# Optimization experiments

Hardware: AMD Instinct MI355X
Metric: run time of the kernel (lower is better)

## Reference

```python
import jax, jax.numpy as jnp
import numpy as np

D_MODEL = 1024
NUM_MODULES = 8
MAX_TRANSLATION = 3.0
MAX_ROT_ANGLE = 3.141592653589793


def setup_inputs() -> dict:
    key = jax.random.key(0)
    k1, k2, k3, k4 = jax.random.split(key, 4)
    B, N = 8, 8192
    node_feats = jax.random.normal(k1, (B, N, D_MODEL), jnp.float32)
    coords = jax.random.normal(k2, (B, N, 3), jnp.float32)
    W = jax.random.normal(k3, (NUM_MODULES * 8, D_MODEL), jnp.float32) * (1.0 / np.sqrt(D_MODEL))
    b = jax.random.normal(k4, (NUM_MODULES * 8,), jnp.float32) * 0.01
    return {"node_feats": node_feats, "coords": coords, "W": W, "b": b}


def _normalize(x, eps=1e-12):
    return x / jnp.clip(jnp.linalg.norm(x, axis=-1, keepdims=True), eps)


def _axis_angle_to_quaternion(aa):
    # pytorch3d convention: quat = [cos(theta/2), axis * sin(theta/2)]
    angles = jnp.linalg.norm(aa, axis=-1, keepdims=True)
    half = angles * 0.5
    small = jnp.abs(angles) < 1e-6
    safe_angles = jnp.where(small, 1.0, angles)
    sin_half_over_angle = jnp.where(small, 0.5 - angles * angles / 48.0, jnp.sin(half) / safe_angles)
    return jnp.concatenate([jnp.cos(half), aa * sin_half_over_angle], axis=-1)


def _quat_mul(a, b):
    aw, ax, ay, az = a[..., 0], a[..., 1], a[..., 2], a[..., 3]
    bw, bx, by, bz = b[..., 0], b[..., 1], b[..., 2], b[..., 3]
    ow = aw * bw - ax * bx - ay * by - az * bz
    ox = aw * bx + ax * bw + ay * bz - az * by
    oy = aw * by - ax * bz + ay * bw + az * bx
    oz = aw * bz + ax * by - ay * bx + az * bw
    return jnp.stack([ow, ox, oy, oz], axis=-1)


def _quat_apply(q, p):
    # q: [B,1,4], p: [B,N,3] -> rotate points: im(q * (0,p) * q^-1)
    pq = jnp.concatenate([jnp.zeros_like(p[..., :1]), p], axis=-1)
    q_inv = q * jnp.array([1.0, -1.0, -1.0, -1.0], q.dtype)
    return _quat_mul(_quat_mul(q, pq), q_inv)[..., 1:]


def reference(node_feats, coords, W, b):
    B, N, _ = coords.shape
    params = (node_feats @ W.T + b).reshape(B, N, NUM_MODULES, 8)
    anchor_logits = params[..., 0:1]   # [B,N,M,1]
    select_logits = params[..., 1:2]
    rot_axis = params[..., 2:5]
    trans = params[..., 5:8]

    anchor_w = jax.nn.softmax(anchor_logits, axis=1)      # softmax over N
    select_p = jax.nn.sigmoid(select_logits)

    angles = jnp.linalg.norm(rot_axis, axis=-1, keepdims=True)
    axis_n = _normalize(rot_axis)
    angles = jnp.tanh(angles) * MAX_ROT_ANGLE
    quats = _axis_angle_to_quaternion(axis_n * angles)    # [B,N,M,4]
    trans = jnp.tanh(trans) * MAX_TRANSLATION             # [B,N,M,3]

    xs = (jnp.moveaxis(quats, 2, 0),     # [M,B,N,4]
          jnp.moveaxis(trans, 2, 0),     # [M,B,N,3]
          jnp.moveaxis(anchor_w, 2, 0),  # [M,B,N,1]
          jnp.moveaxis(select_p, 2, 0))  # [M,B,N,1]

    def step(c, per):
        q, t, aw, sp = per
        anchor = jnp.sum(c * aw, axis=1, keepdims=True)               # [B,1,3]
        s = jnp.clip(jnp.sum(sp, axis=1, keepdims=True), 1e-8)        # [B,1,1]
        q_group = _normalize(jnp.sum(q * sp, axis=1, keepdims=True) / s)  # [B,1,4]
        t_group = jnp.sum(t * sp, axis=1, keepdims=True) / s          # [B,1,3]
        moved = _quat_apply(q_group, c - anchor) + anchor + t_group   # [B,N,3]
        return c + sp * (moved - c), None                             # lerp

    out, _ = jax.lax.scan(step, coords, xs)
    return out
```

## Files before the change

kernel.cpp:

```cpp
#include <hip/hip_runtime.h>
#include <hip/hip_bf16.h>
#include <hip/hip_fp16.h>
#include <math.h>

#define D_MODEL 1024
#define NMOD 8
#define BATCH 8
#define NNODE 8192
#define PI_F 3.14159265358979323846f
#define MAXT 3.0f

typedef short bf16x8 __attribute__((ext_vector_type(8)));
typedef float f32x4 __attribute__((ext_vector_type(4)));

__device__ inline unsigned short f2bf(float x) {
    __hip_bfloat16 h = __float2bfloat16(x);
    return __builtin_bit_cast(unsigned short, h);
}
__device__ inline float h2f(unsigned short u) {
    __half h = __builtin_bit_cast(__half, u);
    return __half2float(h);
}
__device__ inline unsigned short f2h(float x) {
    __half h = __float2half(x);
    return __builtin_bit_cast(unsigned short, h);
}

__global__ void pack_b(const float* __restrict__ W, unsigned short* __restrict__ Bpk) {
    int t = blockIdx.x * 256 + threadIdx.x;
    int l  = t & 63;
    int g  = (t >> 6) & 3;
    int ks = t >> 8;
    int j  = g * 16 + (l & 15);
    int k0 = ks * 32 + ((l >> 4) * 8);
    const float* wp = &W[(size_t)j * D_MODEL + k0];
    bf16x8 pack;
    #pragma unroll
    for (int r = 0; r < 8; ++r) pack[r] = (short)f2bf(wp[r]);
    *reinterpret_cast<bf16x8*>(Bpk + (size_t)t * 8) = pack;
}

__global__ __launch_bounds__(256, 4) void gemm_mfma(
    const float* __restrict__ feats, const unsigned short* __restrict__ Bpk,
    const float* __restrict__ bias,
    unsigned int* __restrict__ esp_out,
    float* __restrict__ sums)
{
    __shared__ float pbuf[4][16][68];
    __shared__ float sacc[64];

    const int tid  = threadIdx.x;
    const int lane = tid & 63;
    const int wv   = tid >> 6;

    if (tid < 64) sacc[tid] = 0.f;
    __syncthreads();

    const int mt    = blockIdx.x * 4 + wv;
    const int mbase = mt * 16;
    const float* arow = feats + (size_t)(mbase + (lane & 15)) * D_MODEL + ((lane >> 4) * 8);
    const bf16x8* bp = reinterpret_cast<const bf16x8*>(Bpk);

    f32x4 acc[4];
    #pragma unroll
    for (int g = 0; g < 4; ++g) acc[g] = (f32x4){0.f, 0.f, 0.f, 0.f};

    #pragma unroll 2
    for (int ks = 0; ks < 32; ++ks) {
        const float4 fa = *reinterpret_cast<const float4*>(arow + ks * 32);
        const float4 fb = *reinterpret_cast<const float4*>(arow + ks * 32 + 4);
        float f[8] = {fa.x, fa.y, fa.z, fa.w, fb.x, fb.y, fb.z, fb.w};
        bf16x8 a;
        #pragma unroll
        for (int i = 0; i < 8; ++i) a[i] = (short)f2bf(f[i]);
        #pragma unroll
        for (int g = 0; g < 4; ++g) {
            bf16x8 bh = bp[(ks * 4 + g) * 64 + lane];
            acc[g] = __builtin_amdgcn_mfma_f32_16x16x32_bf16(a, bh, acc[g], 0, 0, 0);
        }
    }

    #pragma unroll
    for (int g = 0; g < 4; ++g) {
        float bj = bias[g * 16 + (lane & 15)];
        #pragma unroll
        for (int r = 0; r < 4; ++r)
            pbuf[wv][(lane >> 4) * 4 + r][g * 16 + (lane & 15)] = acc[g][r] + bj;
    }

    const int b    = mbase >> 13;
    const int nInB = mbase & 8191;

    #pragma unroll
    for (int h = 0; h < 2; ++h) {
        const int node = lane & 15;
        const int m    = (lane >> 4) + 4 * h;
        const float* pa = &pbuf[wv][node][m * 8];
        float al = pa[0], sl = pa[1];
        float ax = pa[2], ay = pa[3], az = pa[4];
        float tx = pa[5], ty = pa[6], tz = pa[7];

        float ew = expf(al);
        float sp = 1.f / (1.f + expf(-sl));

        float n0  = sqrtf(ax * ax + ay * ay + az * az);
        float inv = 1.f / fmaxf(n0, 1e-12f);
        float ang = tanhf(n0) * PI_F;
        float hf  = 0.5f * ang;
        float shoa = (ang < 1e-6f) ? (0.5f - ang * ang * (1.f / 48.f))
                                   : (sinf(hf) / ang);
        float qw = cosf(hf);
        float fac = inv * ang * shoa;
        float qx = ax * fac, qy = ay * fac, qz = az * fac;

        float ttx = tanhf(tx) * MAXT, tty = tanhf(ty) * MAXT, ttz = tanhf(tz) * MAXT;

        size_t base = ((size_t)(b * NMOD + m)) * NNODE + nInB + node;
        esp_out[base] = ((unsigned)f2h(sp) << 16) | (unsigned)f2h(ew);

        float red[8];
        red[0] = sp;
        red[1] = sp * qw; red[2] = sp * qx; red[3] = sp * qy; red[4] = sp * qz;
        red[5] = sp * ttx; red[6] = sp * tty; red[7] = sp * ttz;
        #pragma unroll
        for (int v = 0; v < 8; ++v) {
            #pragma unroll
            for (int o = 1; o < 16; o <<= 1) red[v] += __shfl_xor(red[v], o);
        }
        if ((lane & 15) == 0) {
            #pragma unroll
            for (int v = 0; v < 8; ++v) atomicAdd(&sacc[m * 8 + v], red[v]);
        }
    }
    __syncthreads();
    if (tid < 64) atomicAdd(&sums[b * 64 + tid], sacc[tid]);
}

__global__ __launch_bounds__(1024) void scan_coords(
    const float* __restrict__ coords,
    const unsigned int* __restrict__ esp_in,
    const float* __restrict__ sums, float* __restrict__ out)
{
    const int b   = blockIdx.x;
    const int tid = threadIdx.x;
    const int lane = tid & 63, wid = tid >> 6;
    __shared__ float redbuf[64];
    __shared__ float bcast[4];

    const int n0 = tid * 8;

    float cx[8], cy[8], cz[8];
    {
        float c[24];
        const float4* cp4 = reinterpret_cast<const float4*>(
            &coords[((size_t)b * NNODE + n0) * 3]);
        #pragma unroll
        for (int q = 0; q < 6; ++q) {
            float4 v = cp4[q];
            c[q * 4 + 0] = v.x; c[q * 4 + 1] = v.y;
            c[q * 4 + 2] = v.z; c[q * 4 + 3] = v.w;
        }
        #pragma unroll
        for (int i = 0; i < 8; ++i) { cx[i] = c[3*i]; cy[i] = c[3*i+1]; cz[i] = c[3*i+2]; }
    }

    const uint4* esp4 = reinterpret_cast<const uint4*>(
        &esp_in[(size_t)b * NMOD * NNODE]);
    uint4 cur0 = esp4[(0 * NNODE + n0) >> 2];
    uint4 cur1 = esp4[((0 * NNODE + n0) >> 2) + 1];

    for (int m = 0; m < NMOD; ++m) {
        const int mn = (m + 1 < NMOD) ? m + 1 : m;
        uint4 nxt0 = esp4[(mn * NNODE + n0) >> 2];
        uint4 nxt1 = esp4[((mn * NNODE + n0) >> 2) + 1];

        unsigned pk[8] = {cur0.x, cur0.y, cur0.z, cur0.w, cur1.x, cur1.y, cur1.z, cur1.w};
        float ev[8], spl[8];
        #pragma unroll
        for (int i = 0; i < 8; ++i) {
            ev[i]  = h2f((unsigned short)(pk[i] & 0xFFFFu));
            spl[i] = h2f((unsigned short)(pk[i] >> 16));
        }

        float se = 0.f, sx = 0.f, sy = 0.f, sz = 0.f;
        #pragma unroll
        for (int i = 0; i < 8; ++i) {
            se += ev[i]; sx += ev[i] * cx[i]; sy += ev[i] * cy[i]; sz += ev[i] * cz[i];
        }
        float vals[4] = {se, sx, sy, sz};
        #pragma unroll
        for (int v = 0; v < 4; ++v) {
            float x = vals[v];
            #pragma unroll
            for (int o = 32; o > 0; o >>= 1) x += __shfl_down(x, o);
            if (lane == 0) redbuf[wid * 4 + v] = x;
        }
        __syncthreads();
        if (wid == 0) {
            float x = redbuf[lane];
            x += __shfl_down(x, 32);
            x += __shfl_down(x, 16);
            x += __shfl_down(x, 8);
            x += __shfl_down(x, 4);
            if (lane < 4) bcast[lane] = x;
        }
        __syncthreads();
        const float SE = bcast[0];
        const float AXc = bcast[1] / SE, AYc = bcast[2] / SE, AZc = bcast[3] / SE;

        const float* sm = &sums[((size_t)b * NMOD + m) * 8];
        float s  = fmaxf(sm[0], 1e-8f);
        float qw = sm[1] / s, qx = sm[2] / s, qy = sm[3] / s, qz = sm[4] / s;
        float qn = sqrtf(qw * qw + qx * qx + qy * qy + qz * qz);
        float qi = 1.f / fmaxf(qn, 1e-12f);
        qw *= qi; qx *= qi; qy *= qi; qz *= qi;
        float tgx = sm[5] / s, tgy = sm[6] / s, tgz = sm[7] / s;

        #pragma unroll
        for (int i = 0; i < 8; ++i) {
            float px = cx[i] - AXc, py = cy[i] - AYc, pz = cz[i] - AZc;
            float ux = qy * pz - qz * py;
            float uy = qz * px - qx * pz;
            float uz = qx * py - qy * px;
            float vx = qy * uz - qz * uy;
            float vy = qz * ux - qx * uz;
            float vz = qx * uy - qy * ux;
            float rx = px + 2.f * (qw * ux + vx);
            float ry = py + 2.f * (qw * uy + vy);
            float rz = pz + 2.f * (qw * uz + vz);
            float mx = rx + AXc + tgx, my = ry + AYc + tgy, mz = rz + AZc + tgz;
            float sp = spl[i];
            cx[i] += sp * (mx - cx[i]);
            cy[i] += sp * (my - cy[i]);
            cz[i] += sp * (mz - cz[i]);
        }
        cur0 = nxt0; cur1 = nxt1;
        __syncthreads();
    }

    {
        float c[24];
        #pragma unroll
        for (int i = 0; i < 8; ++i) { c[3*i] = cx[i]; c[3*i+1] = cy[i]; c[3*i+2] = cz[i]; }
        float4* op4 = reinterpret_cast<float4*>(&out[((size_t)b * NNODE + n0) * 3]);
        #pragma unroll
        for (int q = 0; q < 6; ++q)
            op4[q] = make_float4(c[q*4+0], c[q*4+1], c[q*4+2], c[q*4+3]);
    }
}

extern "C" void kernel_launch(void* const* d_in, const int* in_sizes, int n_in,
                              void* d_out, int out_size, void* d_ws, size_t ws_size,
                              hipStream_t stream) {
    const float* feats  = (const float*)d_in[0];
    const float* coords = (const float*)d_in[1];
    const float* W      = (const float*)d_in[2];
    const float* bias   = (const float*)d_in[3];
    float* out = (float*)d_out;

    char* ws = (char*)d_ws;
    unsigned short* Bpk = (unsigned short*)(ws);
    unsigned int* esp   = (unsigned int*)(ws + 262144);
    float* sums         = (float*)(ws + 262144 + 2097152);

    hipMemsetAsync(sums, 0, (size_t)BATCH * NMOD * 8 * sizeof(float), stream);
    pack_b<<<32, 256, 0, stream>>>(W, Bpk);
    gemm_mfma<<<(BATCH * NNODE) / 64, 256, 0, stream>>>(feats, Bpk, bias, esp, sums);
    scan_coords<<<BATCH, 1024, 0, stream>>>(coords, esp, sums, out);
}
```

Before: 104.6 us.

## Stage packed weights in LDS and double-buffer feature loads in larger GEMM blocks

The GEMM kernel now uses 1024-thread blocks. Each block first copies the whole 128KB packed bf16 weight matrix into LDS with global_load_lds, then streams A rows through two register buffers so the next chunk's loads overlap the current chunk's MFMAs. Weight fragments therefore come from LDS instead of repeated global or L2 reads. The price is 128KB of LDS per block, which limits occupancy to one block per CU, plus a large up-front weight load on each of the 256 blocks and many live registers in the double buffer.

```diff
diff --git a/kernel.cpp b/kernel.cpp
--- a/kernel.cpp
+++ b/kernel.cpp
@@ -40,53 +40,93 @@
     *reinterpret_cast<bf16x8*>(Bpk + (size_t)t * 8) = pack;
 }
 
-__global__ __launch_bounds__(256, 4) void gemm_mfma(
+__device__ __forceinline__ void loadg(float4 (&dst)[8], const float* arow, int g4) {
+    #pragma unroll
+    for (int i = 0; i < 4; ++i) {
+        dst[2 * i]     = *reinterpret_cast<const float4*>(arow + (g4 * 4 + i) * 32);
+        dst[2 * i + 1] = *reinterpret_cast<const float4*>(arow + (g4 * 4 + i) * 32 + 4);
+    }
+}
+
+__device__ __forceinline__ void compg(const float4 (&src)[8], int g4,
+                                      const unsigned short* Blds, int lane,
+                                      f32x4 (&acc)[4]) {
+    #pragma unroll
+    for (int i = 0; i < 4; ++i) {
+        float f[8] = {src[2*i].x, src[2*i].y, src[2*i].z, src[2*i].w,
+                      src[2*i+1].x, src[2*i+1].y, src[2*i+1].z, src[2*i+1].w};
+        bf16x8 a;
+        #pragma unroll
+        for (int j = 0; j < 8; ++j) a[j] = (short)f2bf(f[j]);
+        const int ks = g4 * 4 + i;
+        #pragma unroll
+        for (int g = 0; g < 4; ++g) {
+            bf16x8 bh = *reinterpret_cast<const bf16x8*>(
+                Blds + ((size_t)((ks * 4 + g) * 64 + lane)) * 8);
+            acc[g] = __builtin_amdgcn_mfma_f32_16x16x32_bf16(a, bh, acc[g], 0, 0, 0);
+        }
+    }
+}
+
+__global__ __launch_bounds__(1024) void gemm_mfma(
     const float* __restrict__ feats, const unsigned short* __restrict__ Bpk,
     const float* __restrict__ bias,
     unsigned int* __restrict__ esp_out,
     float* __restrict__ sums)
 {
-    __shared__ float pbuf[4][16][68];
-    __shared__ float sacc[64];
+    __shared__ __align__(16) unsigned char smem[131072];
 
     const int tid  = threadIdx.x;
     const int lane = tid & 63;
     const int wv   = tid >> 6;
 
-    if (tid < 64) sacc[tid] = 0.f;
-    __syncthreads();
-
-    const int mt    = blockIdx.x * 4 + wv;
+    {
+        const char* gsrc = (const char*)Bpk;
+        #pragma unroll
+        for (int r = 0; r < 8; ++r) {
+            const int off = r * 16384 + wv * 1024;
+            __builtin_amdgcn_global_load_lds(
+                (const __attribute__((address_space(1))) unsigned int*)(gsrc + off + lane * 16),
+                (__attribute__((address_space(3))) unsigned int*)(smem + off),
+                16, 0, 0);
+        }
+    }
+
+    const int mt    = blockIdx.x * 16 + wv;
     const int mbase = mt * 16;
     const float* arow = feats + (size_t)(mbase + (lane & 15)) * D_MODEL + ((lane >> 4) * 8);
-    const bf16x8* bp = reinterpret_cast<const bf16x8*>(Bpk);
+    const unsigned short* Blds = (const unsigned short*)smem;
 
     f32x4 acc[4];
     #pragma unroll
     for (int g = 0; g < 4; ++g) acc[g] = (f32x4){0.f, 0.f, 0.f, 0.f};
 
-    #pragma unroll 2
-    for (int ks = 0; ks < 32; ++ks) {
-        const float4 fa = *reinterpret_cast<const float4*>(arow + ks * 32);
-        const float4 fb = *reinterpret_cast<const float4*>(arow + ks * 32 + 4);
-        float f[8] = {fa.x, fa.y, fa.z, fa.w, fb.x, fb.y, fb.z, fb.w};
-        bf16x8 a;
-        #pragma unroll
-        for (int i = 0; i < 8; ++i) a[i] = (short)f2bf(f[i]);
-        #pragma unroll
-        for (int g = 0; g < 4; ++g) {
-            bf16x8 bh = bp[(ks * 4 + g) * 64 + lane];
-            acc[g] = __builtin_amdgcn_mfma_f32_16x16x32_bf16(a, bh, acc[g], 0, 0, 0);
-        }
-    }
+    float4 A0[8], A1[8];
+    loadg(A0, arow, 0);
+    loadg(A1, arow, 1);
+    __syncthreads();
+
+    #pragma unroll
+    for (int g4 = 0; g4 < 8; g4 += 2) {
+        compg(A0, g4, Blds, lane, acc);
+        if (g4 + 2 < 8) loadg(A0, arow, g4 + 2);
+        compg(A1, g4 + 1, Blds, lane, acc);
+        if (g4 + 3 < 8) loadg(A1, arow, g4 + 3);
+    }
+
+    __syncthreads();
+    float* pbuf = reinterpret_cast<float*>(smem) + (size_t)wv * (16 * 68);
+    float* sacc = reinterpret_cast<float*>(smem + 16 * 16 * 68 * 4);
+    if (tid < 64) sacc[tid] = 0.f;
 
     #pragma unroll
     for (int g = 0; g < 4; ++g) {
         float bj = bias[g * 16 + (lane & 15)];
         #pragma unroll
         for (int r = 0; r < 4; ++r)
-            pbuf[wv][(lane >> 4) * 4 + r][g * 16 + (lane & 15)] = acc[g][r] + bj;
-    }
+            pbuf[((lane >> 4) * 4 + r) * 68 + g * 16 + (lane & 15)] = acc[g][r] + bj;
+    }
+    __syncthreads();
 
     const int b    = mbase >> 13;
     const int nInB = mbase & 8191;
@@ -95,7 +135,7 @@
     for (int h = 0; h < 2; ++h) {
         const int node = lane & 15;
         const int m    = (lane >> 4) + 4 * h;
-        const float* pa = &pbuf[wv][node][m * 8];
+        const float* pa = &pbuf[node * 68 + m * 8];
         float al = pa[0], sl = pa[1];
         float ax = pa[2], ay = pa[3], az = pa[4];
         float tx = pa[5], ty = pa[6], tz = pa[7];
@@ -265,6 +305,6 @@
 
     hipMemsetAsync(sums, 0, (size_t)BATCH * NMOD * 8 * sizeof(float), stream);
     pack_b<<<32, 256, 0, stream>>>(W, Bpk);
-    gemm_mfma<<<(BATCH * NNODE) / 64, 256, 0, stream>>>(feats, Bpk, bias, esp, sums);
+    gemm_mfma<<<256, 1024, 0, stream>>>(feats, Bpk, bias, esp, sums);
     scan_coords<<<BATCH, 1024, 0, stream>>>(coords, esp, sums, out);
 }
```

Result: faster. 99.07 us (-5.3%).

## Double-buffer GEMM activation loads, raise occupancy, use rotation matrix in scan

Applied to the files above, without the earlier changes.

The GEMM main loop is restructured into two register buffers that each hold two k-steps of activation loads, with the next loads issued while the current group runs through MFMA. This hides global-load latency on the memory-bound fp32 feature read. The first loads are also hoisted ahead of the shared-memory init barrier. Launch bounds are raised from 4 to 5 blocks per SM for more occupancy. The scan kernel precomputes a 3x3 rotation matrix per module instead of applying the quaternion cross-product form per point, which cuts ALU work. The added registers for prefetch may conflict with the higher occupancy target and could cause spills.

```diff
diff --git a/kernel.cpp b/kernel.cpp
--- a/kernel.cpp
+++ b/kernel.cpp
@@ -40,7 +40,34 @@
     *reinterpret_cast<bf16x8*>(Bpk + (size_t)t * 8) = pack;
 }
 
-__global__ __launch_bounds__(256, 4) void gemm_mfma(
+__device__ __forceinline__ void loadg2(float4 (&dst)[4], const float* arow, int g) {
+    #pragma unroll
+    for (int i = 0; i < 2; ++i) {
+        dst[2 * i]     = *reinterpret_cast<const float4*>(arow + (g * 2 + i) * 32);
+        dst[2 * i + 1] = *reinterpret_cast<const float4*>(arow + (g * 2 + i) * 32 + 4);
+    }
+}
+
+__device__ __forceinline__ void compg2(const float4 (&src)[4], int g,
+                                       const bf16x8* __restrict__ bp, int lane,
+                                       f32x4 (&acc)[4]) {
+    #pragma unroll
+    for (int i = 0; i < 2; ++i) {
+        float f[8] = {src[2*i].x, src[2*i].y, src[2*i].z, src[2*i].w,
+                      src[2*i+1].x, src[2*i+1].y, src[2*i+1].z, src[2*i+1].w};
+        bf16x8 a;
+        #pragma unroll
+        for (int j = 0; j < 8; ++j) a[j] = (short)f2bf(f[j]);
+        const int ks = g * 2 + i;
+        #pragma unroll
+        for (int gg = 0; gg < 4; ++gg) {
+            bf16x8 bh = bp[(ks * 4 + gg) * 64 + lane];
+            acc[gg] = __builtin_amdgcn_mfma_f32_16x16x32_bf16(a, bh, acc[gg], 0, 0, 0);
+        }
+    }
+}
+
+__global__ __launch_bounds__(256, 5) void gemm_mfma(
     const float* __restrict__ feats, const unsigned short* __restrict__ Bpk,
     const float* __restrict__ bias,
     unsigned int* __restrict__ esp_out,
@@ -53,9 +80,6 @@
     const int lane = tid & 63;
     const int wv   = tid >> 6;
 
-    if (tid < 64) sacc[tid] = 0.f;
-    __syncthreads();
-
     const int mt    = blockIdx.x * 4 + wv;
     const int mbase = mt * 16;
     const float* arow = feats + (size_t)(mbase + (lane & 15)) * D_MODEL + ((lane >> 4) * 8);
@@ -65,19 +89,19 @@
     #pragma unroll
     for (int g = 0; g < 4; ++g) acc[g] = (f32x4){0.f, 0.f, 0.f, 0.f};
 
-    #pragma unroll 2
-    for (int ks = 0; ks < 32; ++ks) {
-        const float4 fa = *reinterpret_cast<const float4*>(arow + ks * 32);
-        const float4 fb = *reinterpret_cast<const float4*>(arow + ks * 32 + 4);
-        float f[8] = {fa.x, fa.y, fa.z, fa.w, fb.x, fb.y, fb.z, fb.w};
-        bf16x8 a;
-        #pragma unroll
-        for (int i = 0; i < 8; ++i) a[i] = (short)f2bf(f[i]);
-        #pragma unroll
-        for (int g = 0; g < 4; ++g) {
-            bf16x8 bh = bp[(ks * 4 + g) * 64 + lane];
-            acc[g] = __builtin_amdgcn_mfma_f32_16x16x32_bf16(a, bh, acc[g], 0, 0, 0);
-        }
+    float4 A0[4], A1[4];
+    loadg2(A0, arow, 0);
+    loadg2(A1, arow, 1);
+
+    if (tid < 64) sacc[tid] = 0.f;
+    __syncthreads();
+
+    #pragma unroll
+    for (int g = 0; g < 16; g += 2) {
+        compg2(A0, g, bp, lane, acc);
+        if (g + 2 < 16) loadg2(A0, arow, g + 2);
+        compg2(A1, g + 1, bp, lane, acc);
+        if (g + 3 < 16) loadg2(A1, arow, g + 3);
     }
 
     #pragma unroll
@@ -214,25 +238,25 @@
         float qn = sqrtf(qw * qw + qx * qx + qy * qy + qz * qz);
         float qi = 1.f / fmaxf(qn, 1e-12f);
         qw *= qi; qx *= qi; qy *= qi; qz *= qi;
-        float tgx = sm[5] / s, tgy = sm[6] / s, tgz = sm[7] / s;
+
+        float xx = qx*qx, yy = qy*qy, zz = qz*qz;
+        float xy = qx*qy, xz = qx*qz, yz = qy*qz;
+        float wx = qw*qx, wy = qw*qy, wz = qw*qz;
+        float r00 = 1.f - 2.f*(yy+zz), r01 = 2.f*(xy-wz),       r02 = 2.f*(xz+wy);
+        float r10 = 2.f*(xy+wz),       r11 = 1.f - 2.f*(xx+zz), r12 = 2.f*(yz-wx);
+        float r20 = 2.f*(xz-wy),       r21 = 2.f*(yz+wx),       r22 = 1.f - 2.f*(xx+yy);
+        float dx = AXc + sm[5] / s, dy = AYc + sm[6] / s, dz = AZc + sm[7] / s;
 
         #pragma unroll
         for (int i = 0; i < 8; ++i) {
             float px = cx[i] - AXc, py = cy[i] - AYc, pz = cz[i] - AZc;
-            float ux = qy * pz - qz * py;
-            float uy = qz * px - qx * pz;
-            float uz = qx * py - qy * px;
-            float vx = qy * uz - qz * uy;
-            float vy = qz * ux - qx * uz;
-            float vz = qx * uy - qy * ux;
-            float rx = px + 2.f * (qw * ux + vx);
-            float ry = py + 2.f * (qw * uy + vy);
-            float rz = pz + 2.f * (qw * uz + vz);
-            float mx = rx + AXc + tgx, my = ry + AYc + tgy, mz = rz + AZc + tgz;
+            float mx = fmaf(r00, px, fmaf(r01, py, fmaf(r02, pz, dx)));
+            float my = fmaf(r10, px, fmaf(r11, py, fmaf(r12, pz, dy)));
+            float mz = fmaf(r20, px, fmaf(r21, py, fmaf(r22, pz, dz)));
             float sp = spl[i];
-            cx[i] += sp * (mx - cx[i]);
-            cy[i] += sp * (my - cy[i]);
-            cz[i] += sp * (mz - cz[i]);
+            cx[i] = fmaf(sp, mx - cx[i], cx[i]);
+            cy[i] = fmaf(sp, my - cy[i], cy[i]);
+            cz[i] = fmaf(sp, mz - cz[i], cz[i]);
         }
         cur0 = nxt0; cur1 = nxt1;
         __syncthreads();
```

Measured after the change: 106.1 us. No clear change (+1.4%).
